# Kernel tuning notes

Measured on AMD Instinct MI355X. Metric: run time of the kernel, lower is better.

Reference implementation:

```python
import jax, jax.numpy as jnp
import numpy as np
from jax import lax

B, N_TOK, C_IN, C_OUT = 8, 1024, 128, 256
H_INIT = W_INIT = 32          # init grid; N_TOK == H_INIT*W_INIT (first stage)
N_HEADS, K_NN = 4, 5
CLUSTER_NUM = int(np.ceil(N_TOK * 0.25))  # sample_ratio = 0.25 -> 256


def _grid_index(Hi, Wi, H, W):
    # nearest-neighbor interpolation of flattened map indices (F.interpolate mode='nearest')
    ri = (jnp.arange(Hi) * H) // Hi
    rj = (jnp.arange(Wi) * W) // Wi
    return (ri[:, None] * W + rj[None, :]).reshape(-1)  # [Hi*Wi]


def _map2token(fmap, idx_token):
    # fmap: [B, C, H, W] (H*W < N_init) -> tokens [B, N_TOK, C]; mean over init cells per token
    Bq, C, H, W = fmap.shape
    idx_hw = _grid_index(H_INIT, W_INIT, H, W)                      # [N_init]
    feats = fmap.reshape(Bq, C, H * W)[:, :, idx_hw]                # [B, C, N_init]
    feats = feats.transpose(0, 2, 1).reshape(Bq * H_INIT * W_INIT, C)
    seg = (idx_token + jnp.arange(Bq)[:, None] * N_TOK).reshape(-1)
    num = Bq * N_TOK
    cnt = jax.ops.segment_sum(jnp.ones((Bq * H_INIT * W_INIT,), fmap.dtype), seg, num_segments=num) + 1e-6
    out = jax.ops.segment_sum(feats, seg, num_segments=num)
    return (out / cnt[:, None]).reshape(Bq, N_TOK, C)


def _cdist(a):
    # batched euclidean pairwise distance [B, N, N]
    sq = (a * a).sum(-1)
    d2 = sq[:, :, None] + sq[:, None, :] - 2.0 * jnp.einsum('bnc,bmc->bnm', a, a)
    return jnp.sqrt(jnp.maximum(d2, 0.0))


def _cluster_dpc(x, attn_in, as_out):
    # DPC-KNN clustering (torch version runs under no_grad -> stop_gradient)
    x = lax.stop_gradient(x)
    attn = lax.stop_gradient(attn_in).sum(axis=1)                   # [B, N, N]
    Bq, N, C = x.shape
    scale = 1.0 / jnp.sqrt(jnp.asarray(C, x.dtype))
    dist = 0.8 * (_cdist(x) * scale) + 0.2 * (_cdist(attn) * scale)
    # k nearest distances -> local density
    dist_nearest = -lax.top_k(-dist, K_NN)[0]                       # [B, N, k]
    density = jnp.exp(-(dist_nearest ** 2).mean(-1))                # [B, N]
    density = density + jax.random.uniform(jax.random.key(42), density.shape, density.dtype) * 1e-6
    mask = (density[:, None, :] > density[:, :, None]).astype(x.dtype)
    dist_max = dist.reshape(Bq, -1).max(-1)[:, None, None]
    dmin = (dist * mask + dist_max * (1.0 - mask)).min(-1)          # dist to nearest higher-density point
    score = dmin * density + lax.stop_gradient(as_out).reshape(Bq, -1)
    index_down = lax.top_k(score, CLUSTER_NUM)[1]                   # [B, cluster_num] centers
    dc = jnp.take_along_axis(dist, index_down[:, :, None], axis=1)  # [B, cluster_num, N]
    idx_cluster = dc.argmin(axis=1)                                 # [B, N]
    bidx = jnp.arange(Bq)[:, None]
    idx_cluster = idx_cluster.at[bidx, index_down].set(jnp.broadcast_to(jnp.arange(CLUSTER_NUM)[None, :], index_down.shape))
    return idx_cluster


def _atm_forward(x, attn_in, as_out, conv_w, conv_b, skip_w, ln_g, ln_b, score_w, score_b, idx_token):
    Bq, N, Cin = x.shape
    # TokenConv: pointwise skip + stride-2 conv on the feature map
    x_skip = jnp.einsum('bnc,oc->bno', x, skip_w[:, :, 0])
    x_map = x.reshape(Bq, H_INIT, W_INIT, Cin).transpose(0, 3, 1, 2)  # token2map shortcut (N==N_init==H*W)
    x_map = lax.conv_general_dilated(x_map, conv_w, (2, 2), [(1, 1), (1, 1)],
                                     dimension_numbers=('NCHW', 'OIHW', 'NCHW'))
    x_map = x_map + conv_b[None, :, None, None]                     # [B, C_OUT, 16, 16]
    x1 = x_skip + _map2token(x_map, idx_token)                      # [B, N, C_OUT]
    # LayerNorm
    mu = x1.mean(-1, keepdims=True)
    var = ((x1 - mu) ** 2).mean(-1, keepdims=True)
    xn = (x1 - mu) / jnp.sqrt(var + 1e-5) * ln_g + ln_b
    token_score = xn @ score_w.T + score_b                          # [B, N, 1]
    token_weight = jnp.exp(token_score)
    # DPC-KNN cluster assignment (non-differentiable indices)
    idx_cluster = _cluster_dpc(xn, attn_in, as_out)                 # [B, N]
    # merge_tokens: weighted scatter-mean into cluster slots
    idx = (idx_cluster + jnp.arange(Bq)[:, None] * CLUSTER_NUM).reshape(-1)
    tw = token_weight[..., 0].reshape(-1)
    all_w = jax.ops.segment_sum(tw, idx, num_segments=Bq * CLUSTER_NUM) + 1e-6
    norm_w = tw / all_w[idx]
    src = xn.reshape(Bq * N, C_OUT) * norm_w[:, None]
    x_merged = jax.ops.segment_sum(src, idx, num_segments=Bq * CLUSTER_NUM)
    return x_merged.reshape(Bq, CLUSTER_NUM, C_OUT)


def setup_inputs() -> dict:
    key = jax.random.key(0)
    ks = jax.random.split(key, 6)
    x = jax.random.normal(ks[0], (B, N_TOK, C_IN), jnp.float32)
    attn_in = jax.random.uniform(ks[1], (B, N_HEADS, N_TOK, N_TOK), jnp.float32)
    as_out = jax.random.uniform(ks[2], (B, H_INIT, W_INIT), jnp.float32)
    idx_token = jnp.broadcast_to(jnp.arange(N_TOK), (B, N_TOK))
    agg_weight = jnp.ones((B, N_TOK, 1), jnp.float32)
    conv_w = jax.random.normal(ks[3], (C_OUT, C_IN, 3, 3), jnp.float32) * 0.05
    conv_b = jnp.zeros((C_OUT,), jnp.float32)
    skip_w = jax.random.normal(ks[4], (C_OUT, C_IN, 1), jnp.float32) * 0.05
    ln_g = jnp.ones((C_OUT,), jnp.float32)
    ln_b = jnp.zeros((C_OUT,), jnp.float32)
    score_w = jax.random.normal(ks[5], (1, C_OUT), jnp.float32) * 0.05
    score_b = jnp.zeros((1,), jnp.float32)
    return dict(x=x, attn_in=attn_in, as_out=as_out, conv_w=conv_w, conv_b=conv_b,
                skip_w=skip_w, ln_g=ln_g, ln_b=ln_b, score_w=score_w, score_b=score_b,
                idx_token=idx_token, agg_weight=agg_weight)


def reference(x, attn_in, as_out, conv_w, conv_b, skip_w, ln_g, ln_b, score_w, score_b, idx_token, agg_weight):
    # returns merged token features of the down-sampled dict: [B, CLUSTER_NUM, C_OUT]
    return _atm_forward(x, attn_in, as_out, conv_w, conv_b, skip_w, ln_g, ln_b, score_w, score_b, idx_token)
```

## Files before the change

kernel.cpp:

```cpp
#include <hip/hip_runtime.h>
#include <math.h>

#define BQ 8
#define NT 1024
#define CIN 128
#define CO 256
#define NH 4
#define KNN 5
#define CL 256

__global__ void k_init(float* __restrict__ out, float* __restrict__ acc,
                       float* __restrict__ cnt, float* __restrict__ allw,
                       float* __restrict__ dmax) {
  int i = blockIdx.x * 256 + threadIdx.x;
  acc[i] = 0.f;
  if (i < BQ * CL * CO) out[i] = 0.f;
  if (i < BQ * NT) cnt[i] = 0.f;
  if (i < BQ * CL) allw[i] = 1e-6f;
  if (i < BQ) dmax[i] = 0.f;
}

__global__ void k_headsum(const float4* __restrict__ a, float4* __restrict__ s) {
  int i = blockIdx.x * 256 + threadIdx.x;
  const int per_b = NT * NT / 4;
  int b = i / per_b;
  int rem = i - b * per_b;
  const float4* base = a + (size_t)b * NH * per_b + rem;
  float4 v0 = base[0];
  float4 v1 = base[per_b];
  float4 v2 = base[2 * per_b];
  float4 v3 = base[3 * per_b];
  float4 o;
  o.x = (v0.x + v1.x) + (v2.x + v3.x);
  o.y = (v0.y + v1.y) + (v2.y + v3.y);
  o.z = (v0.z + v1.z) + (v2.z + v3.z);
  o.w = (v0.w + v1.w) + (v2.w + v3.w);
  s[i] = o;
}

__global__ __launch_bounds__(256) void k_conv(const float* __restrict__ x,
                                              const float* __restrict__ w,
                                              const float* __restrict__ bias,
                                              float* __restrict__ xmapT) {
  int blk = blockIdx.x;
  int b = blk >> 8;
  int pq = blk & 255;
  int p = pq >> 4, q = pq & 15;
  __shared__ __align__(16) float patch[CIN * 9];
  for (int e = threadIdx.x; e < CIN * 9; e += 256) {
    int pos = e >> 7;
    int c = e & 127;
    int dy = pos / 3, dx = pos % 3;
    int iy = 2 * p + dy - 1, ix = 2 * q + dx - 1;
    float v = 0.f;
    if (iy >= 0 && iy < 32 && ix >= 0 && ix < 32)
      v = x[((size_t)(b * NT) + iy * 32 + ix) * CIN + c];
    patch[c * 9 + pos] = v;
  }
  __syncthreads();
  int o = threadIdx.x;
  const float* wr = w + (size_t)o * CIN * 9;
  float acc = bias[o];
  for (int e = 0; e < CIN * 9; e += 4) {
    float4 w4 = *(const float4*)(wr + e);
    float4 p4 = *(const float4*)(patch + e);
    acc = fmaf(w4.x, p4.x, acc);
    acc = fmaf(w4.y, p4.y, acc);
    acc = fmaf(w4.z, p4.z, acc);
    acc = fmaf(w4.w, p4.w, acc);
  }
  xmapT[(((size_t)(b << 8) | pq) << 8) + o] = acc;
}

__global__ void k_m2t(const float* __restrict__ xmapT, const int* __restrict__ idx_token,
                      float* __restrict__ acc, float* __restrict__ cnt) {
  int blk = blockIdx.x;
  int b = blk >> 10;
  int cell = blk & 1023;
  int i = cell >> 5, j = cell & 31;
  int cell16 = (i >> 1) * 16 + (j >> 1);
  int t = idx_token[b * NT + cell];
  int o = threadIdx.x;
  float v = xmapT[(((size_t)(b << 8) | cell16) << 8) + o];
  atomicAdd(&acc[((size_t)(b * NT + t) << 8) + o], v);
  if (o == 0) atomicAdd(&cnt[b * NT + t], 1.0f);
}

__global__ __launch_bounds__(256) void k_token(const float* __restrict__ x,
                                               const float* __restrict__ skw,
                                               const float* __restrict__ acc,
                                               const float* __restrict__ cnt,
                                               const float* __restrict__ lng,
                                               const float* __restrict__ lnb,
                                               const float* __restrict__ scw,
                                               const float* __restrict__ scb,
                                               float* __restrict__ xn,
                                               float* __restrict__ tw) {
  int blk = blockIdx.x;
  int b = blk >> 10, n = blk & 1023;
  __shared__ __align__(16) float xrow[CIN];
  __shared__ float red[256];
  int o = threadIdx.x;
  if (o < CIN) xrow[o] = x[(size_t)(b * NT + n) * CIN + o];
  __syncthreads();
  const float* sw = skw + (size_t)o * CIN;
  float s = 0.f;
  for (int c = 0; c < CIN; c += 4) {
    float4 w4 = *(const float4*)(sw + c);
    float4 x4 = *(const float4*)(xrow + c);
    s = fmaf(w4.x, x4.x, s);
    s = fmaf(w4.y, x4.y, s);
    s = fmaf(w4.z, x4.z, s);
    s = fmaf(w4.w, x4.w, s);
  }
  float cdiv = cnt[b * NT + n] + 1e-6f;
  float val = s + acc[((size_t)(b * NT + n) << 8) + o] / cdiv;

  red[o] = val;
  __syncthreads();
  for (int st = 128; st > 0; st >>= 1) { if (o < st) red[o] += red[o + st]; __syncthreads(); }
  float mu = red[0] * (1.0f / 256.0f);
  __syncthreads();
  float d = val - mu;
  red[o] = d * d;
  __syncthreads();
  for (int st = 128; st > 0; st >>= 1) { if (o < st) red[o] += red[o + st]; __syncthreads(); }
  float var = red[0] * (1.0f / 256.0f);
  __syncthreads();
  float xv = d / sqrtf(var + 1e-5f) * lng[o] + lnb[o];
  xn[((size_t)(b * NT + n) << 8) + o] = xv;
  red[o] = xv * scw[o];
  __syncthreads();
  for (int st = 128; st > 0; st >>= 1) { if (o < st) red[o] += red[o + st]; __syncthreads(); }
  if (o == 0) tw[b * NT + n] = expf(red[0] + scb[0]);
}

__global__ void k_sqx(const float* __restrict__ xn, double* __restrict__ sqx) {
  int r = blockIdx.x, t = threadIdx.x;
  __shared__ double red[256];
  float v = xn[((size_t)r << 8) + t];
  red[t] = (double)v * (double)v;
  __syncthreads();
  for (int st = 128; st > 0; st >>= 1) { if (t < st) red[t] += red[t + st]; __syncthreads(); }
  if (t == 0) sqx[r] = red[0];
}

__global__ void k_sqa(const float* __restrict__ asum, double* __restrict__ sqa) {
  int r = blockIdx.x, t = threadIdx.x;
  __shared__ double red[256];
  const float* ar = asum + (size_t)r * NT;
  double s = 0.0;
  for (int k = t; k < NT; k += 256) { float v = ar[k]; s += (double)v * (double)v; }
  red[t] = s;
  __syncthreads();
  for (int st = 128; st > 0; st >>= 1) { if (t < st) red[t] += red[t + st]; __syncthreads(); }
  if (t == 0) sqa[r] = red[0];
}

__global__ __launch_bounds__(256) void k_dist(const float* __restrict__ xn,
                                              const float* __restrict__ asum,
                                              const double* __restrict__ sqx,
                                              const double* __restrict__ sqa,
                                              float* __restrict__ dist) {
  const int b = blockIdx.z;
  const int i0 = blockIdx.y << 6;
  const int j0 = blockIdx.x << 6;
  const int tx = threadIdx.x & 15;
  const int ty = threadIdx.x >> 4;
  __shared__ __align__(16) float At[32 * 68];
  __shared__ __align__(16) float Bt[32 * 68];
  double dxa[4][4], daa[4][4];
#pragma unroll
  for (int r = 0; r < 4; ++r)
#pragma unroll
    for (int c = 0; c < 4; ++c) { dxa[r][c] = 0.0; daa[r][c] = 0.0; }

  const float* xb = xn + (size_t)b * NT * CO;
  for (int kc = 0; kc < CO; kc += 32) {
    for (int e = threadIdx.x; e < 512; e += 256) {
      int rr = e >> 3;
      int gg = e & 7;
      float4 va = *(const float4*)(xb + (size_t)(i0 + rr) * CO + kc + 4 * gg);
      float4 vb = *(const float4*)(xb + (size_t)(j0 + rr) * CO + kc + 4 * gg);
      At[(4 * gg + 0) * 68 + rr] = va.x;
      At[(4 * gg + 1) * 68 + rr] = va.y;
      At[(4 * gg + 2) * 68 + rr] = va.z;
      At[(4 * gg + 3) * 68 + rr] = va.w;
      Bt[(4 * gg + 0) * 68 + rr] = vb.x;
      Bt[(4 * gg + 1) * 68 + rr] = vb.y;
      Bt[(4 * gg + 2) * 68 + rr] = vb.z;
      Bt[(4 * gg + 3) * 68 + rr] = vb.w;
    }
    __syncthreads();
    float f[4][4] = {};
#pragma unroll 8
    for (int kk = 0; kk < 32; ++kk) {
      float4 a4 = *(const float4*)(&At[kk * 68 + (ty << 2)]);
      float4 b4 = *(const float4*)(&Bt[kk * 68 + (tx << 2)]);
      float av[4] = {a4.x, a4.y, a4.z, a4.w};
      float bv[4] = {b4.x, b4.y, b4.z, b4.w};
#pragma unroll
      for (int r = 0; r < 4; ++r)
#pragma unroll
        for (int c = 0; c < 4; ++c) f[r][c] = fmaf(av[r], bv[c], f[r][c]);
    }
#pragma unroll
    for (int r = 0; r < 4; ++r)
#pragma unroll
      for (int c = 0; c < 4; ++c) dxa[r][c] += (double)f[r][c];
    __syncthreads();
  }

  const float* ab = asum + (size_t)b * NT * NT;
  for (int kc = 0; kc < NT; kc += 32) {
    for (int e = threadIdx.x; e < 512; e += 256) {
      int rr = e >> 3;
      int gg = e & 7;
      float4 va = *(const float4*)(ab + (size_t)(i0 + rr) * NT + kc + 4 * gg);
      float4 vb = *(const float4*)(ab + (size_t)(j0 + rr) * NT + kc + 4 * gg);
      At[(4 * gg + 0) * 68 + rr] = va.x;
      At[(4 * gg + 1) * 68 + rr] = va.y;
      At[(4 * gg + 2) * 68 + rr] = va.z;
      At[(4 * gg + 3) * 68 + rr] = va.w;
      Bt[(4 * gg + 0) * 68 + rr] = vb.x;
      Bt[(4 * gg + 1) * 68 + rr] = vb.y;
      Bt[(4 * gg + 2) * 68 + rr] = vb.z;
      Bt[(4 * gg + 3) * 68 + rr] = vb.w;
    }
    __syncthreads();
    float f[4][4] = {};
#pragma unroll 8
    for (int kk = 0; kk < 32; ++kk) {
      float4 a4 = *(const float4*)(&At[kk * 68 + (ty << 2)]);
      float4 b4 = *(const float4*)(&Bt[kk * 68 + (tx << 2)]);
      float av[4] = {a4.x, a4.y, a4.z, a4.w};
      float bv[4] = {b4.x, b4.y, b4.z, b4.w};
#pragma unroll
      for (int r = 0; r < 4; ++r)
#pragma unroll
        for (int c = 0; c < 4; ++c) f[r][c] = fmaf(av[r], bv[c], f[r][c]);
    }
#pragma unroll
    for (int r = 0; r < 4; ++r)
#pragma unroll
      for (int c = 0; c < 4; ++c) daa[r][c] += (double)f[r][c];
    __syncthreads();
  }

  double sxi[4], sai[4], sxj[4], saj[4];
#pragma unroll
  for (int r = 0; r < 4; ++r) {
    sxi[r] = sqx[(size_t)b * NT + i0 + (ty << 2) + r];
    sai[r] = sqa[(size_t)b * NT + i0 + (ty << 2) + r];
  }
#pragma unroll
  for (int c = 0; c < 4; ++c) {
    sxj[c] = sqx[(size_t)b * NT + j0 + (tx << 2) + c];
    saj[c] = sqa[(size_t)b * NT + j0 + (tx << 2) + c];
  }
  const double sc = 0.0625;
#pragma unroll
  for (int r = 0; r < 4; ++r) {
    float4 o4;
    float* op = (float*)&o4;
#pragma unroll
    for (int c = 0; c < 4; ++c) {
      double d2x = sxi[r] + sxj[c] - 2.0 * dxa[r][c];
      double d2a = sai[r] + saj[c] - 2.0 * daa[r][c];
      op[c] = (float)(0.8 * (sqrt(fmax(d2x, 0.0)) * sc) +
                      0.2 * (sqrt(fmax(d2a, 0.0)) * sc));
    }
    *(float4*)&dist[((size_t)b * NT + i0 + (ty << 2) + r) * NT + j0 + (tx << 2)] = o4;
  }
}

__global__ void k_dmax(const float* __restrict__ dist, float* __restrict__ dmax) {
  int b = blockIdx.y;
  __shared__ float red[256];
  float m = 0.f;
  for (size_t idx = (size_t)blockIdx.x * 256 + threadIdx.x; idx < (size_t)NT * NT;
       idx += (size_t)64 * 256)
    m = fmaxf(m, dist[(size_t)b * NT * NT + idx]);
  red[threadIdx.x] = m;
  __syncthreads();
  for (int st = 128; st > 0; st >>= 1) {
    if (threadIdx.x < st) red[threadIdx.x] = fmaxf(red[threadIdx.x], red[threadIdx.x + st]);
    __syncthreads();
  }
  if (threadIdx.x == 0) atomicMax((int*)&dmax[b], __float_as_int(red[0]));
}

__device__ __forceinline__ unsigned rotl32(unsigned x, int d) {
  return (x << d) | (x >> (32 - d));
}
__device__ void threefry2x32(unsigned k0, unsigned k1, unsigned c0, unsigned c1,
                             unsigned* o0, unsigned* o1) {
  unsigned ks2 = k0 ^ k1 ^ 0x1BD11BDAu;
  unsigned x0 = c0 + k0, x1 = c1 + k1;
  const int r0[4] = {13, 15, 26, 6}, r1[4] = {17, 29, 16, 24};
#pragma unroll
  for (int i = 0; i < 4; ++i) { x0 += x1; x1 = rotl32(x1, r0[i]); x1 ^= x0; }
  x0 += k1; x1 += ks2 + 1u;
#pragma unroll
  for (int i = 0; i < 4; ++i) { x0 += x1; x1 = rotl32(x1, r1[i]); x1 ^= x0; }
  x0 += ks2; x1 += k0 + 2u;
#pragma unroll
  for (int i = 0; i < 4; ++i) { x0 += x1; x1 = rotl32(x1, r0[i]); x1 ^= x0; }
  x0 += k0; x1 += k1 + 3u;
#pragma unroll
  for (int i = 0; i < 4; ++i) { x0 += x1; x1 = rotl32(x1, r1[i]); x1 ^= x0; }
  x0 += k1; x1 += ks2 + 4u;
#pragma unroll
  for (int i = 0; i < 4; ++i) { x0 += x1; x1 = rotl32(x1, r0[i]); x1 ^= x0; }
  x0 += ks2; x1 += k0 + 5u;
  *o0 = x0; *o1 = x1;
}

__global__ __launch_bounds__(256) void k_knn(const float* __restrict__ dist,
                                             float* __restrict__ density) {
  int row = blockIdx.x;
  int t = threadIdx.x;
  __shared__ float drow[NT];
  __shared__ float rv[256];
  __shared__ int ri[256];
  float4 v4 = *(const float4*)(dist + (size_t)row * NT + 4 * t);
  drow[4 * t] = v4.x; drow[4 * t + 1] = v4.y;
  drow[4 * t + 2] = v4.z; drow[4 * t + 3] = v4.w;
  __syncthreads();
  float ssum = 0.f;
  for (int r = 0; r < KNN; ++r) {
    float bv = 1e30f;
    int bi = -1;
    for (int k = t; k < NT; k += 256) {
      float v = drow[k];
      if (v < bv || (v == bv && k < bi)) { bv = v; bi = k; }
    }
    rv[t] = bv; ri[t] = bi;
    __syncthreads();
    for (int st = 128; st > 0; st >>= 1) {
      if (t < st) {
        if (rv[t + st] < rv[t] || (rv[t + st] == rv[t] && ri[t + st] < ri[t])) {
          rv[t] = rv[t + st]; ri[t] = ri[t + st];
        }
      }
      __syncthreads();
    }
    if (t == 0) { ssum += rv[0] * rv[0]; drow[ri[0]] = 1e30f; }
    __syncthreads();
  }
  if (t == 0) {
    unsigned i = (unsigned)row;
    unsigned c0 = (i < 4096u) ? i : i - 4096u;
    unsigned c1 = c0 + 4096u;
    unsigned o0, o1;
    threefry2x32(0u, 42u, c0, c1, &o0, &o1);
    unsigned bits = (i < 4096u) ? o0 : o1;
    float u = __uint_as_float((bits >> 9) | 0x3f800000u) - 1.0f;
    density[row] = expf(-(ssum * (1.0f / 5.0f))) + u * 1e-6f;
  }
}

__global__ __launch_bounds__(256) void k_dmin(const float* __restrict__ dist,
                                              const float* __restrict__ density,
                                              const float* __restrict__ as_out,
                                              const float* __restrict__ dmax,
                                              float* __restrict__ score) {
  int row = blockIdx.x;
  int b = row >> 10;
  int i = row & 1023;
  const float* dr = dist + (size_t)row * NT;
  const float* den = density + b * NT;
  float di = den[i];
  float dm = dmax[b];
  __shared__ float red[256];
  float m = dm;
  for (int k = threadIdx.x; k < NT; k += 256) {
    float v = (den[k] > di) ? dr[k] : dm;
    m = fminf(m, v);
  }
  red[threadIdx.x] = m;
  __syncthreads();
  for (int st = 128; st > 0; st >>= 1) {
    if (threadIdx.x < st) red[threadIdx.x] = fminf(red[threadIdx.x], red[threadIdx.x + st]);
    __syncthreads();
  }
  if (threadIdx.x == 0) score[row] = red[0] * di + as_out[row];
}

__global__ __launch_bounds__(1024) void k_topk(const float* __restrict__ score,
                                               int* __restrict__ idx_down) {
  int b = blockIdx.x, t = threadIdx.x;
  __shared__ unsigned long long keys[1024];
  float v = score[b * NT + t];
  unsigned u = __float_as_uint(v);
  u = (u & 0x80000000u) ? ~u : (u | 0x80000000u);
  unsigned inv = ~u;
  keys[t] = ((unsigned long long)inv << 32) | (unsigned)t;
  __syncthreads();
  for (int k = 2; k <= 1024; k <<= 1) {
    for (int j = k >> 1; j > 0; j >>= 1) {
      int ixj = t ^ j;
      if (ixj > t) {
        bool up = ((t & k) == 0);
        unsigned long long a = keys[t], c = keys[ixj];
        if ((a > c) == up) { keys[t] = c; keys[ixj] = a; }
      }
      __syncthreads();
    }
  }
  if (t < CL) idx_down[b * CL + t] = (int)(keys[t] & 0xFFFFFFFFu);
}

__global__ __launch_bounds__(256) void k_assign(const float* __restrict__ dist,
                                                const int* __restrict__ idx_down,
                                                int* __restrict__ idxc) {
  int b = blockIdx.y;
  int n = blockIdx.x * 256 + threadIdx.x;
  __shared__ int cs[CL];
  cs[threadIdx.x] = idx_down[b * CL + threadIdx.x];
  __syncthreads();
  const float* db = dist + (size_t)b * NT * NT;
  float bv = 1e30f;
  int bj = 0;
  for (int j = 0; j < CL; ++j) {
    float v = db[(size_t)cs[j] * NT + n];
    if (v < bv) { bv = v; bj = j; }
  }
  idxc[b * NT + n] = bj;
}

__global__ void k_over(const int* __restrict__ idx_down, int* __restrict__ idxc) {
  int b = blockIdx.x, j = threadIdx.x;
  idxc[b * NT + idx_down[b * CL + j]] = j;
}

__global__ void k_allw(const int* __restrict__ idxc, const float* __restrict__ tw,
                       float* __restrict__ allw) {
  int r = blockIdx.x * 256 + threadIdx.x;
  int b = r >> 10;
  atomicAdd(&allw[b * CL + idxc[r]], tw[r]);
}

__global__ __launch_bounds__(256) void k_merge(const float* __restrict__ xn,
                                               const int* __restrict__ idxc,
                                               const float* __restrict__ tw,
                                               const float* __restrict__ allw,
                                               float* __restrict__ out) {
  int r = blockIdx.x;
  int b = r >> 10;
  int k = idxc[r];
  float w = tw[r] / allw[b * CL + k];
  int o = threadIdx.x;
  atomicAdd(&out[((size_t)(b * CL + k) << 8) + o], xn[((size_t)r << 8) + o] * w);
}

extern "C" void kernel_launch(void* const* d_in, const int* in_sizes, int n_in,
                              void* d_out, int out_size, void* d_ws, size_t ws_size,
                              hipStream_t stream) {
  (void)in_sizes; (void)n_in; (void)out_size; (void)ws_size;
  const float* x       = (const float*)d_in[0];
  const float* attn    = (const float*)d_in[1];
  const float* as_out  = (const float*)d_in[2];
  const float* conv_w  = (const float*)d_in[3];
  const float* conv_b  = (const float*)d_in[4];
  const float* skip_w  = (const float*)d_in[5];
  const float* ln_g    = (const float*)d_in[6];
  const float* ln_b    = (const float*)d_in[7];
  const float* score_w = (const float*)d_in[8];
  const float* score_b = (const float*)d_in[9];
  const int*   idx_tok = (const int*)d_in[10];
  float* out = (float*)d_out;

  char* p = (char*)d_ws;
  float*  asum    = (float*)(p);
  float*  dist    = (float*)(p + 33554432);
  float*  xmapT   = (float*)(p + 67108864);
  float*  acc     = (float*)(p + 69206016);
  float*  cnt     = (float*)(p + 77594624);
  float*  xn      = (float*)(p + 77627392);
  float*  tw      = (float*)(p + 86016000);
  double* sqx     = (double*)(p + 86048768);
  double* sqa     = (double*)(p + 86114304);
  float*  density = (float*)(p + 86179840);
  float*  score   = (float*)(p + 86212608);
  float*  dmax    = (float*)(p + 86245376);
  int*    idxdown = (int*)(p + 86245632);
  int*    idxc    = (int*)(p + 86253824);
  float*  allw    = (float*)(p + 86286592);

  k_init<<<8192, 256, 0, stream>>>(out, acc, cnt, allw, dmax);
  k_headsum<<<8192, 256, 0, stream>>>((const float4*)attn, (float4*)asum);
  k_conv<<<2048, 256, 0, stream>>>(x, conv_w, conv_b, xmapT);
  k_m2t<<<8192, 256, 0, stream>>>(xmapT, idx_tok, acc, cnt);
  k_token<<<8192, 256, 0, stream>>>(x, skip_w, acc, cnt, ln_g, ln_b, score_w, score_b, xn, tw);
  k_sqx<<<8192, 256, 0, stream>>>(xn, sqx);
  k_sqa<<<8192, 256, 0, stream>>>(asum, sqa);
  k_dist<<<dim3(16, 16, 8), 256, 0, stream>>>(xn, asum, sqx, sqa, dist);
  k_dmax<<<dim3(64, 8), 256, 0, stream>>>(dist, dmax);
  k_knn<<<8192, 256, 0, stream>>>(dist, density);
  k_dmin<<<8192, 256, 0, stream>>>(dist, density, as_out, dmax, score);
  k_topk<<<8, 1024, 0, stream>>>(score, idxdown);
  k_assign<<<dim3(4, 8), 256, 0, stream>>>(dist, idxdown, idxc);
  k_over<<<8, 256, 0, stream>>>(idxdown, idxc);
  k_allw<<<32, 256, 0, stream>>>(idxc, tw, allw);
  k_merge<<<8192, 256, 0, stream>>>(xn, idxc, tw, allw, out);
}
```

Baseline: 971.4 us.

## Fuse norms into producers, compute symmetric distance tiles once, fold dmax into dist

```diff
diff --git a/kernel.cpp b/kernel.cpp
--- a/kernel.cpp
+++ b/kernel.cpp
@@ -20,8 +20,12 @@
   if (i < BQ) dmax[i] = 0.f;
 }
 
-__global__ void k_headsum(const float4* __restrict__ a, float4* __restrict__ s) {
-  int i = blockIdx.x * 256 + threadIdx.x;
+__global__ __launch_bounds__(256) void k_headsum_sqa(const float4* __restrict__ a,
+                                                     float4* __restrict__ s,
+                                                     double* __restrict__ sqa) {
+  int blk = blockIdx.x;
+  int t = threadIdx.x;
+  int i = blk * 256 + t;
   const int per_b = NT * NT / 4;
   int b = i / per_b;
   int rem = i - b * per_b;
@@ -36,6 +40,12 @@
   o.z = (v0.z + v1.z) + (v2.z + v3.z);
   o.w = (v0.w + v1.w) + (v2.w + v3.w);
   s[i] = o;
+  __shared__ double red[256];
+  red[t] = ((double)o.x * (double)o.x + (double)o.y * (double)o.y) +
+           ((double)o.z * (double)o.z + (double)o.w * (double)o.w);
+  __syncthreads();
+  for (int st = 128; st > 0; st >>= 1) { if (t < st) red[t] += red[t + st]; __syncthreads(); }
+  if (t == 0) sqa[blk] = red[0];
 }
 
 __global__ __launch_bounds__(256) void k_conv(const float* __restrict__ x,
@@ -95,11 +105,13 @@
                                                const float* __restrict__ scw,
                                                const float* __restrict__ scb,
                                                float* __restrict__ xn,
+                                               double* __restrict__ sqx,
                                                float* __restrict__ tw) {
   int blk = blockIdx.x;
   int b = blk >> 10, n = blk & 1023;
   __shared__ __align__(16) float xrow[CIN];
   __shared__ float red[256];
+  __shared__ double redd[256];
   int o = threadIdx.x;
   if (o < CIN) xrow[o] = x[(size_t)(b * NT + n) * CIN + o];
   __syncthreads();
@@ -129,46 +141,40 @@
   __syncthreads();
   float xv = d / sqrtf(var + 1e-5f) * lng[o] + lnb[o];
   xn[((size_t)(b * NT + n) << 8) + o] = xv;
+  redd[o] = (double)xv * (double)xv;
+  __syncthreads();
+  for (int st = 128; st > 0; st >>= 1) { if (o < st) redd[o] += redd[o + st]; __syncthreads(); }
+  if (o == 0) sqx[b * NT + n] = redd[0];
+  __syncthreads();
   red[o] = xv * scw[o];
   __syncthreads();
   for (int st = 128; st > 0; st >>= 1) { if (o < st) red[o] += red[o + st]; __syncthreads(); }
   if (o == 0) tw[b * NT + n] = expf(red[0] + scb[0]);
 }
 
-__global__ void k_sqx(const float* __restrict__ xn, double* __restrict__ sqx) {
-  int r = blockIdx.x, t = threadIdx.x;
-  __shared__ double red[256];
-  float v = xn[((size_t)r << 8) + t];
-  red[t] = (double)v * (double)v;
-  __syncthreads();
-  for (int st = 128; st > 0; st >>= 1) { if (t < st) red[t] += red[t + st]; __syncthreads(); }
-  if (t == 0) sqx[r] = red[0];
-}
-
-__global__ void k_sqa(const float* __restrict__ asum, double* __restrict__ sqa) {
-  int r = blockIdx.x, t = threadIdx.x;
-  __shared__ double red[256];
-  const float* ar = asum + (size_t)r * NT;
-  double s = 0.0;
-  for (int k = t; k < NT; k += 256) { float v = ar[k]; s += (double)v * (double)v; }
-  red[t] = s;
-  __syncthreads();
-  for (int st = 128; st > 0; st >>= 1) { if (t < st) red[t] += red[t + st]; __syncthreads(); }
-  if (t == 0) sqa[r] = red[0];
-}
-
-__global__ __launch_bounds__(256) void k_dist(const float* __restrict__ xn,
-                                              const float* __restrict__ asum,
-                                              const double* __restrict__ sqx,
-                                              const double* __restrict__ sqa,
-                                              float* __restrict__ dist) {
-  const int b = blockIdx.z;
-  const int i0 = blockIdx.y << 6;
-  const int j0 = blockIdx.x << 6;
-  const int tx = threadIdx.x & 15;
-  const int ty = threadIdx.x >> 4;
-  __shared__ __align__(16) float At[32 * 68];
-  __shared__ __align__(16) float Bt[32 * 68];
+__global__ __launch_bounds__(256) void k_dist_tri(const float* __restrict__ xn,
+                                                  const float* __restrict__ asum,
+                                                  const double* __restrict__ sqx,
+                                                  const double* __restrict__ sqa,
+                                                  float* __restrict__ dist,
+                                                  float* __restrict__ dmax) {
+  const int b = blockIdx.y;
+  int rem = blockIdx.x;
+  int ti = 0;
+  while (rem >= 16 - ti) { rem -= 16 - ti; ++ti; }
+  const int tj = ti + rem;
+  const int i0 = ti << 6;
+  const int j0 = tj << 6;
+  const int t = threadIdx.x;
+  const int tx = t & 15;
+  const int ty = t >> 4;
+  const int rr = t >> 3;
+  const int gg = t & 7;
+
+  __shared__ __align__(16) float SM[4352];
+  float* At = SM;
+  float* Bt = SM + 2176;
+
   double dxa[4][4], daa[4][4];
 #pragma unroll
   for (int r = 0; r < 4; ++r)
@@ -176,22 +182,33 @@
     for (int c = 0; c < 4; ++c) { dxa[r][c] = 0.0; daa[r][c] = 0.0; }
 
   const float* xb = xn + (size_t)b * NT * CO;
+  float4 pa0 = *(const float4*)(xb + (size_t)(i0 + rr) * CO + 4 * gg);
+  float4 pa1 = *(const float4*)(xb + (size_t)(i0 + rr + 32) * CO + 4 * gg);
+  float4 pb0 = *(const float4*)(xb + (size_t)(j0 + rr) * CO + 4 * gg);
+  float4 pb1 = *(const float4*)(xb + (size_t)(j0 + rr + 32) * CO + 4 * gg);
   for (int kc = 0; kc < CO; kc += 32) {
-    for (int e = threadIdx.x; e < 512; e += 256) {
-      int rr = e >> 3;
-      int gg = e & 7;
-      float4 va = *(const float4*)(xb + (size_t)(i0 + rr) * CO + kc + 4 * gg);
-      float4 vb = *(const float4*)(xb + (size_t)(j0 + rr) * CO + kc + 4 * gg);
-      At[(4 * gg + 0) * 68 + rr] = va.x;
-      At[(4 * gg + 1) * 68 + rr] = va.y;
-      At[(4 * gg + 2) * 68 + rr] = va.z;
-      At[(4 * gg + 3) * 68 + rr] = va.w;
-      Bt[(4 * gg + 0) * 68 + rr] = vb.x;
-      Bt[(4 * gg + 1) * 68 + rr] = vb.y;
-      Bt[(4 * gg + 2) * 68 + rr] = vb.z;
-      Bt[(4 * gg + 3) * 68 + rr] = vb.w;
-    }
-    __syncthreads();
+    At[(4 * gg + 0) * 68 + rr] = pa0.x;
+    At[(4 * gg + 1) * 68 + rr] = pa0.y;
+    At[(4 * gg + 2) * 68 + rr] = pa0.z;
+    At[(4 * gg + 3) * 68 + rr] = pa0.w;
+    At[(4 * gg + 0) * 68 + rr + 32] = pa1.x;
+    At[(4 * gg + 1) * 68 + rr + 32] = pa1.y;
+    At[(4 * gg + 2) * 68 + rr + 32] = pa1.z;
+    At[(4 * gg + 3) * 68 + rr + 32] = pa1.w;
+    Bt[(4 * gg + 0) * 68 + rr] = pb0.x;
+    Bt[(4 * gg + 1) * 68 + rr] = pb0.y;
+    Bt[(4 * gg + 2) * 68 + rr] = pb0.z;
+    Bt[(4 * gg + 3) * 68 + rr] = pb0.w;
+    Bt[(4 * gg + 0) * 68 + rr + 32] = pb1.x;
+    Bt[(4 * gg + 1) * 68 + rr + 32] = pb1.y;
+    Bt[(4 * gg + 2) * 68 + rr + 32] = pb1.z;
+    Bt[(4 * gg + 3) * 68 + rr + 32] = pb1.w;
+    __syncthreads();
+    int kn = (kc + 32 < CO) ? kc + 32 : 0;
+    pa0 = *(const float4*)(xb + (size_t)(i0 + rr) * CO + kn + 4 * gg);
+    pa1 = *(const float4*)(xb + (size_t)(i0 + rr + 32) * CO + kn + 4 * gg);
+    pb0 = *(const float4*)(xb + (size_t)(j0 + rr) * CO + kn + 4 * gg);
+    pb1 = *(const float4*)(xb + (size_t)(j0 + rr + 32) * CO + kn + 4 * gg);
     float f[4][4] = {};
 #pragma unroll 8
     for (int kk = 0; kk < 32; ++kk) {
@@ -212,22 +229,33 @@
   }
 
   const float* ab = asum + (size_t)b * NT * NT;
+  pa0 = *(const float4*)(ab + (size_t)(i0 + rr) * NT + 4 * gg);
+  pa1 = *(const float4*)(ab + (size_t)(i0 + rr + 32) * NT + 4 * gg);
+  pb0 = *(const float4*)(ab + (size_t)(j0 + rr) * NT + 4 * gg);
+  pb1 = *(const float4*)(ab + (size_t)(j0 + rr + 32) * NT + 4 * gg);
   for (int kc = 0; kc < NT; kc += 32) {
-    for (int e = threadIdx.x; e < 512; e += 256) {
-      int rr = e >> 3;
-      int gg = e & 7;
-      float4 va = *(const float4*)(ab + (size_t)(i0 + rr) * NT + kc + 4 * gg);
-      float4 vb = *(const float4*)(ab + (size_t)(j0 + rr) * NT + kc + 4 * gg);
-      At[(4 * gg + 0) * 68 + rr] = va.x;
-      At[(4 * gg + 1) * 68 + rr] = va.y;
-      At[(4 * gg + 2) * 68 + rr] = va.z;
-      At[(4 * gg + 3) * 68 + rr] = va.w;
-      Bt[(4 * gg + 0) * 68 + rr] = vb.x;
-      Bt[(4 * gg + 1) * 68 + rr] = vb.y;
-      Bt[(4 * gg + 2) * 68 + rr] = vb.z;
-      Bt[(4 * gg + 3) * 68 + rr] = vb.w;
-    }
-    __syncthreads();
+    At[(4 * gg + 0) * 68 + rr] = pa0.x;
+    At[(4 * gg + 1) * 68 + rr] = pa0.y;
+    At[(4 * gg + 2) * 68 + rr] = pa0.z;
+    At[(4 * gg + 3) * 68 + rr] = pa0.w;
+    At[(4 * gg + 0) * 68 + rr + 32] = pa1.x;
+    At[(4 * gg + 1) * 68 + rr + 32] = pa1.y;
+    At[(4 * gg + 2) * 68 + rr + 32] = pa1.z;
+    At[(4 * gg + 3) * 68 + rr + 32] = pa1.w;
+    Bt[(4 * gg + 0) * 68 + rr] = pb0.x;
+    Bt[(4 * gg + 1) * 68 + rr] = pb0.y;
+    Bt[(4 * gg + 2) * 68 + rr] = pb0.z;
+    Bt[(4 * gg + 3) * 68 + rr] = pb0.w;
+    Bt[(4 * gg + 0) * 68 + rr + 32] = pb1.x;
+    Bt[(4 * gg + 1) * 68 + rr + 32] = pb1.y;
+    Bt[(4 * gg + 2) * 68 + rr + 32] = pb1.z;
+    Bt[(4 * gg + 3) * 68 + rr + 32] = pb1.w;
+    __syncthreads();
+    int kn = (kc + 32 < NT) ? kc + 32 : 0;
+    pa0 = *(const float4*)(ab + (size_t)(i0 + rr) * NT + kn + 4 * gg);
+    pa1 = *(const float4*)(ab + (size_t)(i0 + rr + 32) * NT + kn + 4 * gg);
+    pb0 = *(const float4*)(ab + (size_t)(j0 + rr) * NT + kn + 4 * gg);
+    pb1 = *(const float4*)(ab + (size_t)(j0 + rr + 32) * NT + kn + 4 * gg);
     float f[4][4] = {};
 #pragma unroll 8
     for (int kk = 0; kk < 32; ++kk) {
@@ -259,35 +287,44 @@
     saj[c] = sqa[(size_t)b * NT + j0 + (tx << 2) + c];
   }
   const double sc = 0.0625;
+  float ov[4][4];
+  float mx = 0.f;
 #pragma unroll
   for (int r = 0; r < 4; ++r) {
-    float4 o4;
-    float* op = (float*)&o4;
 #pragma unroll
     for (int c = 0; c < 4; ++c) {
       double d2x = sxi[r] + sxj[c] - 2.0 * dxa[r][c];
       double d2a = sai[r] + saj[c] - 2.0 * daa[r][c];
-      op[c] = (float)(0.8 * (sqrt(fmax(d2x, 0.0)) * sc) +
-                      0.2 * (sqrt(fmax(d2a, 0.0)) * sc));
-    }
+      float v = (float)(0.8 * (sqrt(fmax(d2x, 0.0)) * sc) +
+                        0.2 * (sqrt(fmax(d2a, 0.0)) * sc));
+      ov[r][c] = v;
+      mx = fmaxf(mx, v);
+    }
+    float4 o4 = {ov[r][0], ov[r][1], ov[r][2], ov[r][3]};
     *(float4*)&dist[((size_t)b * NT + i0 + (ty << 2) + r) * NT + j0 + (tx << 2)] = o4;
   }
-}
-
-__global__ void k_dmax(const float* __restrict__ dist, float* __restrict__ dmax) {
-  int b = blockIdx.y;
-  __shared__ float red[256];
-  float m = 0.f;
-  for (size_t idx = (size_t)blockIdx.x * 256 + threadIdx.x; idx < (size_t)NT * NT;
-       idx += (size_t)64 * 256)
-    m = fmaxf(m, dist[(size_t)b * NT * NT + idx]);
-  red[threadIdx.x] = m;
-  __syncthreads();
-  for (int st = 128; st > 0; st >>= 1) {
-    if (threadIdx.x < st) red[threadIdx.x] = fmaxf(red[threadIdx.x], red[threadIdx.x + st]);
-    __syncthreads();
-  }
-  if (threadIdx.x == 0) atomicMax((int*)&dmax[b], __float_as_int(red[0]));
+
+  if (ti != tj) {
+    float* tile = SM;
+#pragma unroll
+    for (int r = 0; r < 4; ++r)
+#pragma unroll
+      for (int c = 0; c < 4; ++c)
+        tile[((ty << 2) + r) * 65 + (tx << 2) + c] = ov[r][c];
+    __syncthreads();
+#pragma unroll
+    for (int r = 0; r < 4; ++r) {
+      float4 o4;
+      o4.x = tile[((tx << 2) + 0) * 65 + (ty << 2) + r];
+      o4.y = tile[((tx << 2) + 1) * 65 + (ty << 2) + r];
+      o4.z = tile[((tx << 2) + 2) * 65 + (ty << 2) + r];
+      o4.w = tile[((tx << 2) + 3) * 65 + (ty << 2) + r];
+      *(float4*)&dist[((size_t)b * NT + j0 + (ty << 2) + r) * NT + i0 + (tx << 2)] = o4;
+    }
+  }
+
+  for (int off = 32; off > 0; off >>= 1) mx = fmaxf(mx, __shfl_xor(mx, off));
+  if ((t & 63) == 0) atomicMax((int*)&dmax[b], __float_as_int(mx));
 }
 
 __device__ __forceinline__ unsigned rotl32(unsigned x, int d) {
@@ -321,8 +358,8 @@
   int row = blockIdx.x;
   int t = threadIdx.x;
   __shared__ float drow[NT];
-  __shared__ float rv[256];
-  __shared__ int ri[256];
+  __shared__ float wv[4];
+  __shared__ int wi[4];
   float4 v4 = *(const float4*)(dist + (size_t)row * NT + 4 * t);
   drow[4 * t] = v4.x; drow[4 * t + 1] = v4.y;
   drow[4 * t + 2] = v4.z; drow[4 * t + 3] = v4.w;
@@ -330,22 +367,27 @@
   float ssum = 0.f;
   for (int r = 0; r < KNN; ++r) {
     float bv = 1e30f;
-    int bi = -1;
+    int bi = NT;
     for (int k = t; k < NT; k += 256) {
       float v = drow[k];
       if (v < bv || (v == bv && k < bi)) { bv = v; bi = k; }
     }
-    rv[t] = bv; ri[t] = bi;
-    __syncthreads();
-    for (int st = 128; st > 0; st >>= 1) {
-      if (t < st) {
-        if (rv[t + st] < rv[t] || (rv[t + st] == rv[t] && ri[t + st] < ri[t])) {
-          rv[t] = rv[t + st]; ri[t] = ri[t + st];
-        }
-      }
-      __syncthreads();
-    }
-    if (t == 0) { ssum += rv[0] * rv[0]; drow[ri[0]] = 1e30f; }
+    for (int off = 32; off > 0; off >>= 1) {
+      float ov = __shfl_xor(bv, off);
+      int oi = __shfl_xor(bi, off);
+      if (ov < bv || (ov == bv && oi < bi)) { bv = ov; bi = oi; }
+    }
+    if ((t & 63) == 0) { wv[t >> 6] = bv; wi[t >> 6] = bi; }
+    __syncthreads();
+    bv = wv[0]; bi = wi[0];
+#pragma unroll
+    for (int w2 = 1; w2 < 4; ++w2) {
+      float ov = wv[w2];
+      int oi = wi[w2];
+      if (ov < bv || (ov == bv && oi < bi)) { bv = ov; bi = oi; }
+    }
+    ssum += bv * bv;
+    if (t == 0) drow[bi] = 1e30f;
     __syncthreads();
   }
   if (t == 0) {
@@ -489,14 +531,12 @@
   float*  allw    = (float*)(p + 86286592);
 
   k_init<<<8192, 256, 0, stream>>>(out, acc, cnt, allw, dmax);
-  k_headsum<<<8192, 256, 0, stream>>>((const float4*)attn, (float4*)asum);
+  k_headsum_sqa<<<8192, 256, 0, stream>>>((const float4*)attn, (float4*)asum, sqa);
   k_conv<<<2048, 256, 0, stream>>>(x, conv_w, conv_b, xmapT);
   k_m2t<<<8192, 256, 0, stream>>>(xmapT, idx_tok, acc, cnt);
-  k_token<<<8192, 256, 0, stream>>>(x, skip_w, acc, cnt, ln_g, ln_b, score_w, score_b, xn, tw);
-  k_sqx<<<8192, 256, 0, stream>>>(xn, sqx);
-  k_sqa<<<8192, 256, 0, stream>>>(asum, sqa);
-  k_dist<<<dim3(16, 16, 8), 256, 0, stream>>>(xn, asum, sqx, sqa, dist);
-  k_dmax<<<dim3(64, 8), 256, 0, stream>>>(dist, dmax);
+  k_token<<<8192, 256, 0, stream>>>(x, skip_w, acc, cnt, ln_g, ln_b, score_w, score_b,
+                                    xn, sqx, tw);
+  k_dist_tri<<<dim3(136, 8), 256, 0, stream>>>(xn, asum, sqx, sqa, dist, dmax);
   k_knn<<<8192, 256, 0, stream>>>(dist, density);
   k_dmin<<<8192, 256, 0, stream>>>(dist, density, as_out, dmax, score);
   k_topk<<<8, 1024, 0, stream>>>(score, idxdown);
```

Result: faster. 801.7 us (median of 2 runs) (-17.5%).
